# Performance work log

Hardware: AMD Instinct MI355X
Metric: run time of the kernel (lower is better)

Reference implementation:

```python
import jax, jax.numpy as jnp
import numpy as np

N_NODES = 50000


def setup_inputs() -> dict:
    key = jax.random.key(0)
    k1, k2, k3, k4, k5 = jax.random.split(key, 5)
    h = jax.random.normal(k1, (50000, 256), dtype=jnp.float32)
    norm = jax.random.uniform(k2, (50000, 1), dtype=jnp.float32)
    weight = jax.random.normal(k3, (256, 96), dtype=jnp.float32) * (1.0 / np.sqrt(96.0))
    src = jax.random.randint(k4, (800000,), 0, N_NODES, dtype=jnp.int64)
    dst = jax.random.randint(k5, (800000,), 0, N_NODES, dtype=jnp.int64)
    return {"h": h, "norm": norm, "weight": weight, "src": src, "dst": dst}


def reference(h, norm, weight, src, dst):
    # dense projection: [N, in] @ [in, out] -> [N, out]
    hw = jnp.matmul(h, weight)
    # pre-aggregation degree norm
    hw = hw * norm
    # copy_src + sum: gather messages from src, scatter-add into dst
    msgs = hw[src]  # [E, out]
    agg = jax.ops.segment_sum(msgs, dst, num_segments=N_NODES)
    # post-aggregation degree norm + activation
    out = jax.nn.relu(agg * norm)
    return out
```

## Files before the change

kernel.cpp:

```cpp
#include <hip/hip_runtime.h>

#define M_NODES 50000
#define KDIM    256
#define NDIM    96
#define NEDGE   800000
#define BM      64
#define GEMM_BLKS 782
#define NPB     64
#define NBUCK   782
#define CAPB    1536
#define EPB     2048
#define NBLK_SC 391

typedef short bf16x8 __attribute__((ext_vector_type(8)));
typedef float f32x4  __attribute__((ext_vector_type(4)));

__device__ inline unsigned short f2bf(float x) {
    unsigned u = __float_as_uint(x);
    u = (u + 0x7fffu + ((u >> 16) & 1u)) >> 16;
    return (unsigned short)u;
}
__device__ inline unsigned pack2bf(float x, float y) {
    return (unsigned)f2bf(x) | ((unsigned)f2bf(y) << 16);
}

__global__ __launch_bounds__(256) void prep_w_kernel(
    const float* __restrict__ w, unsigned short* __restrict__ wt,
    int* __restrict__ gcursor)
{
    const int b = blockIdx.x, t = threadIdx.x;
    if (b < 96) {
        wt[b * 256 + t] = f2bf(w[(size_t)t * NDIM + b]);
    } else {
        for (int i = t; i < NBUCK; i += 256) gcursor[i] = i * CAPB;
    }
}

__global__ __launch_bounds__(256) void gemm_mfma_kernel(
    const float* __restrict__ h, const float* __restrict__ norm,
    const unsigned short* __restrict__ wt, unsigned short* __restrict__ hwb)
{
    __shared__ __align__(16) char smem[81920];

    const int tid = threadIdx.x;
    char* w_lds = smem;
    char* a_lds = smem + 49152;
    const int lane = tid & 63;
    const int wv   = tid >> 6;
    const int row0 = blockIdx.x * BM;

#pragma unroll
    for (int it = 0; it < 8; ++it) {
        int idx = tid + it * 256;
        int r   = idx >> 5;
        int u   = idx & 31;
        int row = row0 + r;
        if (row >= M_NODES) row = M_NODES - 1;
        const float* hp = h + (size_t)row * KDIM + u * 8;
        float4 p = *reinterpret_cast<const float4*>(hp);
        float4 q = *reinterpret_cast<const float4*>(hp + 4);
        uint4 o;
        o.x = pack2bf(p.x, p.y); o.y = pack2bf(p.z, p.w);
        o.z = pack2bf(q.x, q.y); o.w = pack2bf(q.z, q.w);
        *reinterpret_cast<uint4*>(a_lds + r * 512 + ((u * 16) ^ ((r & 7) << 4))) = o;
    }
#pragma unroll
    for (int it = 0; it < 12; ++it) {
        int idx = tid + it * 256;
        int n   = idx >> 5;
        int kb  = (idx & 31) * 16;
        uint4 v = *reinterpret_cast<const uint4*>(
            reinterpret_cast<const char*>(wt) + n * 512 + kb);
        *reinterpret_cast<uint4*>(w_lds + n * 512 + (kb ^ ((n & 7) << 4))) = v;
    }
    __syncthreads();

    f32x4 acc[6];
#pragma unroll
    for (int f = 0; f < 6; ++f) acc[f] = (f32x4){0.f, 0.f, 0.f, 0.f};

    const int ar = wv * 16 + (lane & 15);
    const int kg = lane >> 4;

#pragma unroll
    for (int s = 0; s < 8; ++s) {
        const int kb = s * 64 + kg * 16;
        bf16x8 a = *reinterpret_cast<const bf16x8*>(
            a_lds + ar * 512 + (kb ^ ((ar & 7) << 4)));
#pragma unroll
        for (int f = 0; f < 6; ++f) {
            int n = f * 16 + (lane & 15);
            bf16x8 b = *reinterpret_cast<const bf16x8*>(
                w_lds + n * 512 + (kb ^ ((n & 7) << 4)));
            acc[f] = __builtin_amdgcn_mfma_f32_16x16x32_bf16(a, b, acc[f], 0, 0, 0);
        }
    }

    const int crow = wv * 16 + (lane >> 4) * 4;
    const int ccol = lane & 15;
#pragma unroll
    for (int r = 0; r < 4; ++r) {
        int row = row0 + crow + r;
        if (row < M_NODES) {
            float nv = norm[row];
#pragma unroll
            for (int f = 0; f < 6; ++f)
                hwb[(size_t)row * NDIM + f * 16 + ccol] = f2bf(acc[f][r] * nv);
        }
    }
}

__global__ __launch_bounds__(256) void bin_scatter_kernel(
    const int* __restrict__ src, const int* __restrict__ dst,
    int* __restrict__ gcursor, unsigned* __restrict__ binned)
{
    __shared__ int s_cnt[NBUCK];
    __shared__ int s_base[NBUCK];
    const int tid = threadIdx.x;
    const int e0 = blockIdx.x * EPB;
    const int e1 = (e0 + EPB < NEDGE) ? e0 + EPB : NEDGE;

    for (int i = tid; i < NBUCK; i += 256) s_cnt[i] = 0;
    __syncthreads();
    for (int e = e0 + tid; e < e1; e += 256)
        atomicAdd(&s_cnt[dst[e] >> 6], 1);
    __syncthreads();
    for (int i = tid; i < NBUCK; i += 256) {
        int c = s_cnt[i];
        s_base[i] = c ? atomicAdd(&gcursor[i], c) : 0;
    }
    __syncthreads();
    for (int i = tid; i < NBUCK; i += 256) s_cnt[i] = 0;
    __syncthreads();
    for (int e = e0 + tid; e < e1; e += 256) {
        int d = dst[e];
        int b = d >> 6;
        int pos = s_base[b] + atomicAdd(&s_cnt[b], 1);
        if (pos < (b + 1) * CAPB)
            binned[pos] = ((unsigned)(d & 63) << 16) | (unsigned)src[e];
    }
}

#define ACCV(A, v)                                     \
    A[0] += __uint_as_float((v).x << 16);              \
    A[1] += __uint_as_float((v).x & 0xffff0000u);      \
    A[2] += __uint_as_float((v).y << 16);              \
    A[3] += __uint_as_float((v).y & 0xffff0000u);      \
    A[4] += __uint_as_float((v).z << 16);              \
    A[5] += __uint_as_float((v).z & 0xffff0000u);      \
    A[6] += __uint_as_float((v).w << 16);              \
    A[7] += __uint_as_float((v).w & 0xffff0000u);

__global__ __launch_bounds__(768) void csr_agg_kernel(
    const unsigned* __restrict__ binned, const int* __restrict__ gcursor,
    const unsigned short* __restrict__ hwb, const float* __restrict__ norm,
    float* __restrict__ out)
{
    __shared__ unsigned eL[CAPB];
    __shared__ unsigned short oL[CAPB];
    __shared__ int cnt[NPB];
    __shared__ int pfxE[NPB];

    const int b  = blockIdx.x;
    const int t  = threadIdx.x;
    const int e0 = b * CAPB;
    int cntE = gcursor[b] - e0;
    if (cntE > CAPB) cntE = CAPB;

    for (int i = t; i < cntE; i += 768) eL[i] = binned[e0 + i];
    if (t < NPB) cnt[t] = 0;
    __syncthreads();
    for (int i = t; i < cntE; i += 768)
        atomicAdd(&cnt[(eL[i] >> 16) & 63], 1);
    __syncthreads();
    if (t < NPB) {
        int v = cnt[t];
        int x = v;
#pragma unroll
        for (int st = 1; st < 64; st <<= 1) {
            int o = __shfl_up(x, st, 64);
            if (t >= st) x += o;
        }
        int ex = x - v;
        pfxE[t] = ex;
        cnt[t]  = ex;
    }
    __syncthreads();
    for (int i = t; i < cntE; i += 768) {
        unsigned v = eL[i];
        int d = (v >> 16) & 63;
        int p = atomicAdd(&cnt[d], 1);
        oL[p] = (unsigned short)(v & 0xffffu);
    }
    __syncthreads();

    const int node  = t / 12;
    const int c8    = t - node * 12;
    const int gnode = b * NPB + node;
    if (gnode < M_NODES) {
        const int s0 = pfxE[node];
        const int s1 = cnt[node];
        float acc[8]  = {0.f, 0.f, 0.f, 0.f, 0.f, 0.f, 0.f, 0.f};
        float acc2[8] = {0.f, 0.f, 0.f, 0.f, 0.f, 0.f, 0.f, 0.f};
        int e = s0;
        for (; e + 4 <= s1; e += 4) {
            int a0 = oL[e], a1 = oL[e + 1], a2 = oL[e + 2], a3 = oL[e + 3];
            uint4 v0 = *reinterpret_cast<const uint4*>(hwb + (size_t)a0 * NDIM + c8 * 8);
            uint4 v1 = *reinterpret_cast<const uint4*>(hwb + (size_t)a1 * NDIM + c8 * 8);
            uint4 v2 = *reinterpret_cast<const uint4*>(hwb + (size_t)a2 * NDIM + c8 * 8);
            uint4 v3 = *reinterpret_cast<const uint4*>(hwb + (size_t)a3 * NDIM + c8 * 8);
            ACCV(acc, v0); ACCV(acc2, v1); ACCV(acc, v2); ACCV(acc2, v3);
        }
        for (; e < s1; ++e) {
            int a0 = oL[e];
            uint4 v0 = *reinterpret_cast<const uint4*>(hwb + (size_t)a0 * NDIM + c8 * 8);
            ACCV(acc, v0);
        }
        const float nv = norm[gnode];
        float4 o0, o1;
        o0.x = fmaxf((acc[0] + acc2[0]) * nv, 0.f);
        o0.y = fmaxf((acc[1] + acc2[1]) * nv, 0.f);
        o0.z = fmaxf((acc[2] + acc2[2]) * nv, 0.f);
        o0.w = fmaxf((acc[3] + acc2[3]) * nv, 0.f);
        o1.x = fmaxf((acc[4] + acc2[4]) * nv, 0.f);
        o1.y = fmaxf((acc[5] + acc2[5]) * nv, 0.f);
        o1.z = fmaxf((acc[6] + acc2[6]) * nv, 0.f);
        o1.w = fmaxf((acc[7] + acc2[7]) * nv, 0.f);
        float4* po = reinterpret_cast<float4*>(out + (size_t)gnode * NDIM + c8 * 8);
        po[0] = o0; po[1] = o1;
    }
}

extern "C" void kernel_launch(void* const* d_in, const int* in_sizes, int n_in,
                              void* d_out, int out_size, void* d_ws, size_t ws_size,
                              hipStream_t stream)
{
    const float* h    = (const float*)d_in[0];
    const float* norm = (const float*)d_in[1];
    const float* w    = (const float*)d_in[2];
    const int*   src  = (const int*)d_in[3];
    const int*   dst  = (const int*)d_in[4];
    float* out = (float*)d_out;

    unsigned short* hwb = (unsigned short*)d_ws;
    unsigned short* wt  = hwb + (size_t)M_NODES * NDIM;
    int* gcursor = (int*)(wt + KDIM * NDIM);
    unsigned* binned = (unsigned*)(gcursor + 800);

    prep_w_kernel<<<97, 256, 0, stream>>>(w, wt, gcursor);
    bin_scatter_kernel<<<NBLK_SC, 256, 0, stream>>>(src, dst, gcursor, binned);
    gemm_mfma_kernel<<<GEMM_BLKS, 256, 0, stream>>>(h, norm, wt, hwb);
    csr_agg_kernel<<<NBUCK, 768, 0, stream>>>(binned, gcursor, hwb, norm, out);
}
```

Measured before the change: 73.19 us.

## Fuse GEMM and edge binning into one heterogeneous launch

Merges the bf16 MFMA projection kernel and the edge bin-scatter kernel into a single launch. Even blocks run the GEMM and odd blocks run the scatter, so the two independent stages overlap on the GPU and one launch gap disappears. Each GEMM block now covers two 64-row tiles and loads W into LDS once for both. Each wave stages its own A slice, so no block barrier is needed per tile. The cost is that scatter blocks reserve the GEMM's 80KB of LDS, which lowers their occupancy, and each GEMM block carries more serial work.

```diff
diff --git a/kernel.cpp b/kernel.cpp
--- a/kernel.cpp
+++ b/kernel.cpp
@@ -5,12 +5,14 @@
 #define NDIM    96
 #define NEDGE   800000
 #define BM      64
-#define GEMM_BLKS 782
+#define TPB     2
+#define GEMM_BLKS 391
 #define NPB     64
 #define NBUCK   782
 #define CAPB    1536
 #define EPB     2048
 #define NBLK_SC 391
+#define TOT_BLKS 782
 
 typedef short bf16x8 __attribute__((ext_vector_type(8)));
 typedef float f32x4  __attribute__((ext_vector_type(4)));
@@ -36,108 +38,115 @@
     }
 }
 
-__global__ __launch_bounds__(256) void gemm_mfma_kernel(
+__global__ __launch_bounds__(256) void fused_gemm_scatter_kernel(
     const float* __restrict__ h, const float* __restrict__ norm,
-    const unsigned short* __restrict__ wt, unsigned short* __restrict__ hwb)
-{
-    __shared__ __align__(16) char smem[81920];
-
-    const int tid = threadIdx.x;
-    char* w_lds = smem;
-    char* a_lds = smem + 49152;
-    const int lane = tid & 63;
-    const int wv   = tid >> 6;
-    const int row0 = blockIdx.x * BM;
-
-#pragma unroll
-    for (int it = 0; it < 8; ++it) {
-        int idx = tid + it * 256;
-        int r   = idx >> 5;
-        int u   = idx & 31;
-        int row = row0 + r;
-        if (row >= M_NODES) row = M_NODES - 1;
-        const float* hp = h + (size_t)row * KDIM + u * 8;
-        float4 p = *reinterpret_cast<const float4*>(hp);
-        float4 q = *reinterpret_cast<const float4*>(hp + 4);
-        uint4 o;
-        o.x = pack2bf(p.x, p.y); o.y = pack2bf(p.z, p.w);
-        o.z = pack2bf(q.x, q.y); o.w = pack2bf(q.z, q.w);
-        *reinterpret_cast<uint4*>(a_lds + r * 512 + ((u * 16) ^ ((r & 7) << 4))) = o;
-    }
-#pragma unroll
-    for (int it = 0; it < 12; ++it) {
-        int idx = tid + it * 256;
-        int n   = idx >> 5;
-        int kb  = (idx & 31) * 16;
-        uint4 v = *reinterpret_cast<const uint4*>(
-            reinterpret_cast<const char*>(wt) + n * 512 + kb);
-        *reinterpret_cast<uint4*>(w_lds + n * 512 + (kb ^ ((n & 7) << 4))) = v;
-    }
-    __syncthreads();
-
-    f32x4 acc[6];
-#pragma unroll
-    for (int f = 0; f < 6; ++f) acc[f] = (f32x4){0.f, 0.f, 0.f, 0.f};
-
-    const int ar = wv * 16 + (lane & 15);
-    const int kg = lane >> 4;
-
-#pragma unroll
-    for (int s = 0; s < 8; ++s) {
-        const int kb = s * 64 + kg * 16;
-        bf16x8 a = *reinterpret_cast<const bf16x8*>(
-            a_lds + ar * 512 + (kb ^ ((ar & 7) << 4)));
-#pragma unroll
-        for (int f = 0; f < 6; ++f) {
-            int n = f * 16 + (lane & 15);
-            bf16x8 b = *reinterpret_cast<const bf16x8*>(
-                w_lds + n * 512 + (kb ^ ((n & 7) << 4)));
-            acc[f] = __builtin_amdgcn_mfma_f32_16x16x32_bf16(a, b, acc[f], 0, 0, 0);
-        }
-    }
-
-    const int crow = wv * 16 + (lane >> 4) * 4;
-    const int ccol = lane & 15;
-#pragma unroll
-    for (int r = 0; r < 4; ++r) {
-        int row = row0 + crow + r;
-        if (row < M_NODES) {
-            float nv = norm[row];
-#pragma unroll
-            for (int f = 0; f < 6; ++f)
-                hwb[(size_t)row * NDIM + f * 16 + ccol] = f2bf(acc[f][r] * nv);
-        }
-    }
-}
-
-__global__ __launch_bounds__(256) void bin_scatter_kernel(
+    const unsigned short* __restrict__ wt, unsigned short* __restrict__ hwb,
     const int* __restrict__ src, const int* __restrict__ dst,
     int* __restrict__ gcursor, unsigned* __restrict__ binned)
 {
-    __shared__ int s_cnt[NBUCK];
-    __shared__ int s_base[NBUCK];
+    __shared__ __align__(16) char smem[81920];
+
     const int tid = threadIdx.x;
-    const int e0 = blockIdx.x * EPB;
-    const int e1 = (e0 + EPB < NEDGE) ? e0 + EPB : NEDGE;
-
-    for (int i = tid; i < NBUCK; i += 256) s_cnt[i] = 0;
-    __syncthreads();
-    for (int e = e0 + tid; e < e1; e += 256)
-        atomicAdd(&s_cnt[dst[e] >> 6], 1);
-    __syncthreads();
-    for (int i = tid; i < NBUCK; i += 256) {
-        int c = s_cnt[i];
-        s_base[i] = c ? atomicAdd(&gcursor[i], c) : 0;
-    }
-    __syncthreads();
-    for (int i = tid; i < NBUCK; i += 256) s_cnt[i] = 0;
-    __syncthreads();
-    for (int e = e0 + tid; e < e1; e += 256) {
-        int d = dst[e];
-        int b = d >> 6;
-        int pos = s_base[b] + atomicAdd(&s_cnt[b], 1);
-        if (pos < (b + 1) * CAPB)
-            binned[pos] = ((unsigned)(d & 63) << 16) | (unsigned)src[e];
+    const unsigned bx = blockIdx.x;
+
+    if ((bx & 1) == 0) {
+        const int g = (int)(bx >> 1);
+        char* w_lds = smem;
+        char* a_lds = smem + 49152 + (tid >> 6) * 8192;
+        const int lane = tid & 63;
+        const int wv   = tid >> 6;
+
+#pragma unroll
+        for (int it = 0; it < 12; ++it) {
+            int idx = tid + it * 256;
+            int n   = idx >> 5;
+            int kb  = (idx & 31) * 16;
+            uint4 v = *reinterpret_cast<const uint4*>(
+                reinterpret_cast<const char*>(wt) + n * 512 + kb);
+            *reinterpret_cast<uint4*>(w_lds + n * 512 + (kb ^ ((n & 7) << 4))) = v;
+        }
+        __syncthreads();
+
+        const int r16 = lane & 15;
+        const int kg  = lane >> 4;
+
+        for (int t = 0; t < TPB; ++t) {
+            const int row0 = g * (BM * TPB) + t * BM + wv * 16;
+
+#pragma unroll
+            for (int it = 0; it < 8; ++it) {
+                int flat = it * 64 + lane;
+                int r    = flat >> 5;
+                int u    = flat & 31;
+                int grow = row0 + r;
+                if (grow >= M_NODES) grow = M_NODES - 1;
+                const float* hp = h + (size_t)grow * KDIM + u * 8;
+                float4 p = *reinterpret_cast<const float4*>(hp);
+                float4 q = *reinterpret_cast<const float4*>(hp + 4);
+                uint4 o;
+                o.x = pack2bf(p.x, p.y); o.y = pack2bf(p.z, p.w);
+                o.z = pack2bf(q.x, q.y); o.w = pack2bf(q.z, q.w);
+                *reinterpret_cast<uint4*>(
+                    a_lds + r * 512 + ((u * 16) ^ ((r & 7) << 4))) = o;
+            }
+
+            f32x4 acc[6];
+#pragma unroll
+            for (int f = 0; f < 6; ++f) acc[f] = (f32x4){0.f, 0.f, 0.f, 0.f};
+
+#pragma unroll
+            for (int s = 0; s < 8; ++s) {
+                const int kb = s * 64 + kg * 16;
+                bf16x8 a = *reinterpret_cast<const bf16x8*>(
+                    a_lds + r16 * 512 + (kb ^ ((r16 & 7) << 4)));
+#pragma unroll
+                for (int f = 0; f < 6; ++f) {
+                    int n = f * 16 + (lane & 15);
+                    bf16x8 b = *reinterpret_cast<const bf16x8*>(
+                        w_lds + n * 512 + (kb ^ ((n & 7) << 4)));
+                    acc[f] = __builtin_amdgcn_mfma_f32_16x16x32_bf16(a, b, acc[f], 0, 0, 0);
+                }
+            }
+
+            const int crow = row0 + (lane >> 4) * 4;
+            const int ccol = lane & 15;
+#pragma unroll
+            for (int r = 0; r < 4; ++r) {
+                int row = crow + r;
+                if (row < M_NODES) {
+                    float nv = norm[row];
+#pragma unroll
+                    for (int f = 0; f < 6; ++f)
+                        hwb[(size_t)row * NDIM + f * 16 + ccol] = f2bf(acc[f][r] * nv);
+                }
+            }
+        }
+    } else {
+        int* s_cnt  = reinterpret_cast<int*>(smem);
+        int* s_base = s_cnt + NBUCK;
+        const int blk = (int)(bx >> 1);
+        const int e0 = blk * EPB;
+        const int e1 = (e0 + EPB < NEDGE) ? e0 + EPB : NEDGE;
+
+        for (int i = tid; i < NBUCK; i += 256) s_cnt[i] = 0;
+        __syncthreads();
+        for (int e = e0 + tid; e < e1; e += 256)
+            atomicAdd(&s_cnt[dst[e] >> 6], 1);
+        __syncthreads();
+        for (int i = tid; i < NBUCK; i += 256) {
+            int c = s_cnt[i];
+            s_base[i] = c ? atomicAdd(&gcursor[i], c) : 0;
+        }
+        __syncthreads();
+        for (int i = tid; i < NBUCK; i += 256) s_cnt[i] = 0;
+        __syncthreads();
+        for (int e = e0 + tid; e < e1; e += 256) {
+            int d = dst[e];
+            int b = d >> 6;
+            int pos = s_base[b] + atomicAdd(&s_cnt[b], 1);
+            if (pos < (b + 1) * CAPB)
+                binned[pos] = ((unsigned)(d & 63) << 16) | (unsigned)src[e];
+        }
     }
 }
 
@@ -248,7 +257,7 @@
     unsigned* binned = (unsigned*)(gcursor + 800);
 
     prep_w_kernel<<<97, 256, 0, stream>>>(w, wt, gcursor);
-    bin_scatter_kernel<<<NBLK_SC, 256, 0, stream>>>(src, dst, gcursor, binned);
-    gemm_mfma_kernel<<<GEMM_BLKS, 256, 0, stream>>>(h, norm, wt, hwb);
+    fused_gemm_scatter_kernel<<<TOT_BLKS, 256, 0, stream>>>(
+        h, norm, wt, hwb, src, dst, gcursor, binned);
     csr_agg_kernel<<<NBUCK, 768, 0, stream>>>(binned, gcursor, hwb, norm, out);
 }
```

New measurement: 63.34 us, median of 2. 1.16x faster.
